# Kernel tuning notes

Measured on AMD Instinct MI355X. Metric: run time of the kernel, lower is better.

The kernel has to match this reference:

```python
import jax, jax.numpy as jnp
import numpy as np

N = 100000   # nodes
E = 1600000  # edges
D = 128      # input feature dim
H = 128      # hidden dim
C = 40       # output classes


def _gcn_conv(x, W, b, src, dst, norm):
    # PyG GCNConv: h = x @ W; out_i = sum_j (d_i^-1/2 d_j^-1/2) h_j over in-edges,
    # including self-loops, then + bias. norm = deg^-1/2 with self-loop-augmented degree.
    h = x @ W                                    # [N, H]
    coef = norm[src] * norm[dst]                 # [E]
    agg = jax.ops.segment_sum(h[src] * coef[:, None], dst, num_segments=N)
    agg = agg + h * (norm * norm)[:, None]       # self-loop term
    return agg + b


def setup_inputs() -> dict:
    key = jax.random.key(0)
    ks = jax.random.split(key, 12)
    x = jax.random.normal(ks[0], (N, D), dtype=jnp.float32)
    edge_index = jax.random.randint(ks[1], (2, E), 0, N, dtype=jnp.int64)

    def lin(k, fan_in, fan_out):
        s = 1.0 / np.sqrt(fan_in)
        return jax.random.uniform(k, (fan_in, fan_out), jnp.float32, -s, s)

    return {
        "x": x,
        "edge_index": edge_index,
        "W1": lin(ks[2], D, H), "b1": jnp.zeros((H,), jnp.float32),
        "W2": lin(ks[3], H, H), "b2": jnp.zeros((H,), jnp.float32),
        "W3": lin(ks[4], H, H), "b3": jnp.zeros((H,), jnp.float32),
        "Wp1": lin(ks[5], H, H), "bp1": jnp.zeros((H,), jnp.float32),
        "Wp2": lin(ks[6], H, C), "bp2": jnp.zeros((C,), jnp.float32),
    }


def reference(x, edge_index, W1, b1, W2, b2, W3, b3, Wp1, bp1, Wp2, bp2):
    src, dst = edge_index[0], edge_index[1]
    # degree with self-loops (GCNConv adds self-loops by default)
    deg = jax.ops.segment_sum(jnp.ones((E,), jnp.float32), dst, num_segments=N) + 1.0
    norm = jax.lax.rsqrt(deg)                    # deg^-1/2

    h = x
    for W, b in ((W1, b1), (W2, b2), (W3, b3)):
        h = _gcn_conv(h, W, b, src, dst, norm)
        h = jax.nn.relu(h)
        # dropout is a no-op at inference / rate 0

    h = h @ Wp1 + bp1
    h = h @ Wp2 + bp2
    return jax.nn.log_softmax(h, axis=1)
```

## Files before the change

kernel.cpp:

```cpp
#include <hip/hip_runtime.h>
#include <hip/hip_bf16.h>
#include <math.h>


#define DH 128
#define NC 40
#define BN 128
#define MAXNB 1024
#define CAP 2560
#define CH 4096
#define SP 136
#define NPREP (3 * DH * DH + 48 * DH + 48)

typedef __attribute__((ext_vector_type(8))) short bf16x8;
typedef __attribute__((ext_vector_type(4))) float f32x4;

__device__ __forceinline__ unsigned short f2bf(float f) {
    unsigned u = __float_as_uint(f);
    unsigned r = (u + 0x7fffu + ((u >> 16) & 1u)) >> 16;
    return (unsigned short)r;
}
__device__ __forceinline__ unsigned pack2(float lo, float hi) {
    return (unsigned)f2bf(lo) | ((unsigned)f2bf(hi) << 16);
}


__global__ __launch_bounds__(256) void bucket_scatter_prep(
        const int* __restrict__ src, const int* __restrict__ dst, int E,
        unsigned* __restrict__ bpos, unsigned* __restrict__ ebuf,
        const float* __restrict__ W1, const float* __restrict__ W2,
        const float* __restrict__ W3, const float* __restrict__ Wp1,
        const float* __restrict__ bp1, const float* __restrict__ Wp2,
        const float* __restrict__ bp2, unsigned short* __restrict__ Wt,
        unsigned short* __restrict__ Wft, float* __restrict__ bfh, int gC) {
    __shared__ unsigned hist[MAXNB];
    __shared__ unsigned gbase[MAXNB];
    __shared__ unsigned lim[MAXNB];
    __shared__ unsigned cur[MAXNB];
    const int tid = threadIdx.x;

    if (blockIdx.x >= gC) {
        int id = (blockIdx.x - gC) * 256 + tid;
        if (id < 3 * DH * DH) {
            int l = id >> 14, r = id & (DH * DH - 1);
            int k = r >> 7, n = r & 127;
            const float* W = (l == 0) ? W1 : (l == 1) ? W2 : W3;
            Wt[l * DH * DH + n * DH + k] = f2bf(W[k * DH + n]);
        } else if (id < 3 * DH * DH + 48 * DH) {
            int o = id - 3 * DH * DH;
            int c = o >> 7, k = o & 127;
            float acc = 0.f;
            if (c < NC)
                for (int j = 0; j < DH; ++j) acc += Wp1[k * DH + j] * Wp2[j * NC + c];
            Wft[c * DH + k] = f2bf(acc);
        } else if (id < NPREP) {
            int c = id - 3 * DH * DH - 48 * DH;
            float acc = 0.f;
            if (c < NC) {
                acc = bp2[c];
                for (int j = 0; j < DH; ++j) acc += bp1[j] * Wp2[j * NC + c];
            }
            bfh[c] = acc;
        }
        return;
    }

    const int e0 = blockIdx.x * CH;
    const int nE = min(CH, E - e0);
    const int nE4 = nE & ~3;

    for (int i = tid; i < MAXNB; i += 256) { hist[i] = 0; cur[i] = 0; }
    __syncthreads();
    for (int i = tid * 4; i < nE4; i += 1024) {
        int4 dv = *(const int4*)(dst + e0 + i);
        atomicAdd(&hist[(unsigned)dv.x >> 7], 1u);
        atomicAdd(&hist[(unsigned)dv.y >> 7], 1u);
        atomicAdd(&hist[(unsigned)dv.z >> 7], 1u);
        atomicAdd(&hist[(unsigned)dv.w >> 7], 1u);
    }
    for (int i = nE4 + tid; i < nE; i += 256)
        atomicAdd(&hist[(unsigned)dst[e0 + i] >> 7], 1u);
    __syncthreads();
    for (int i = tid; i < MAXNB; i += 256) {
        unsigned h = hist[i];
        if (h) {
            unsigned o = (unsigned)i * CAP + atomicAdd(&bpos[i], h);
            gbase[i] = o;
            lim[i] = min(o + h, (unsigned)(i + 1) * CAP);
        }
    }
    __syncthreads();
    for (int i = tid * 4; i < nE4; i += 1024) {
        int4 sv = *(const int4*)(src + e0 + i);
        int4 dv = *(const int4*)(dst + e0 + i);
        {
            unsigned b = (unsigned)dv.x >> 7;
            unsigned p = gbase[b] + atomicAdd(&cur[b], 1u);
            if (p < lim[b]) ebuf[p] = ((unsigned)sv.x << 7) | ((unsigned)dv.x & 127u);
        }
        {
            unsigned b = (unsigned)dv.y >> 7;
            unsigned p = gbase[b] + atomicAdd(&cur[b], 1u);
            if (p < lim[b]) ebuf[p] = ((unsigned)sv.y << 7) | ((unsigned)dv.y & 127u);
        }
        {
            unsigned b = (unsigned)dv.z >> 7;
            unsigned p = gbase[b] + atomicAdd(&cur[b], 1u);
            if (p < lim[b]) ebuf[p] = ((unsigned)sv.z << 7) | ((unsigned)dv.z & 127u);
        }
        {
            unsigned b = (unsigned)dv.w >> 7;
            unsigned p = gbase[b] + atomicAdd(&cur[b], 1u);
            if (p < lim[b]) ebuf[p] = ((unsigned)sv.w << 7) | ((unsigned)dv.w & 127u);
        }
    }
    for (int i = nE4 + tid; i < nE; i += 256) {
        int s = src[e0 + i];
        int d = dst[e0 + i];
        unsigned b = (unsigned)d >> 7;
        unsigned p = gbase[b] + atomicAdd(&cur[b], 1u);
        if (p < lim[b]) ebuf[p] = ((unsigned)s << 7) | ((unsigned)d & 127u);
    }
}


__global__ __launch_bounds__(256) void bucket_degfill(const unsigned* __restrict__ ebuf,
                                                      const unsigned* __restrict__ bpos,
                                                      unsigned* __restrict__ cnt,
                                                      float* __restrict__ nrm,
                                                      unsigned* __restrict__ offN,
                                                      unsigned* __restrict__ dh,
                                                      int* __restrict__ csr, int N) {
    __shared__ unsigned h[BN], lb[BN], cur[BN];
    __shared__ int lcsr[CAP];
    __shared__ unsigned dhh[256];
    __shared__ unsigned tot;

    int b = blockIdx.x, tid = threadIdx.x;
    unsigned ebase = (unsigned)b * CAP;
    unsigned used = min(bpos[b], (unsigned)CAP);
    unsigned used4 = used & ~3u;

    if (tid < BN) { h[tid] = 0; cur[tid] = 0; }
    dhh[tid] = 0;
    if (tid == 0) tot = 0;
    __syncthreads();

    for (unsigned i = tid * 4; i < used4; i += 1024) {
        uint4 v = *(const uint4*)(ebuf + ebase + i);
        atomicAdd(&h[v.x & 127u], 1u);
        atomicAdd(&h[v.y & 127u], 1u);
        atomicAdd(&h[v.z & 127u], 1u);
        atomicAdd(&h[v.w & 127u], 1u);
    }
    for (unsigned i = used4 + tid; i < used; i += 256)
        atomicAdd(&h[ebuf[ebase + i] & 127u], 1u);
    __syncthreads();

    if (tid < BN) {
        unsigned m = h[tid];
        lb[tid] = m ? atomicAdd(&tot, m) : 0u;
    }
    __syncthreads();

    for (unsigned i = tid * 4; i < used4; i += 1024) {
        uint4 v = *(const uint4*)(ebuf + ebase + i);
        {
            unsigned nl = v.x & 127u;
            unsigned r = atomicAdd(&cur[nl], 1u);
            lcsr[lb[nl] + r] = (int)(v.x >> 7);
        }
        {
            unsigned nl = v.y & 127u;
            unsigned r = atomicAdd(&cur[nl], 1u);
            lcsr[lb[nl] + r] = (int)(v.y >> 7);
        }
        {
            unsigned nl = v.z & 127u;
            unsigned r = atomicAdd(&cur[nl], 1u);
            lcsr[lb[nl] + r] = (int)(v.z >> 7);
        }
        {
            unsigned nl = v.w & 127u;
            unsigned r = atomicAdd(&cur[nl], 1u);
            lcsr[lb[nl] + r] = (int)(v.w >> 7);
        }
    }
    for (unsigned i = used4 + tid; i < used; i += 256) {
        unsigned v = ebuf[ebase + i];
        unsigned nl = v & 127u;
        unsigned r = atomicAdd(&cur[nl], 1u);
        lcsr[lb[nl] + r] = (int)(v >> 7);
    }

    if (tid < BN) {
        int node = b * BN + tid;
        if (node < N) {
            unsigned m = h[tid];
            cnt[node] = m;
            nrm[node] = rsqrtf((float)m + 1.0f);
            offN[node] = ebase + lb[tid];
            atomicAdd(&dhh[min(m, 255u)], 1u);
        }
    }
    __syncthreads();

    for (unsigned i = tid * 4; i < used4; i += 1024)
        *(int4*)(csr + ebase + i) = *(const int4*)&lcsr[i];
    for (unsigned i = used4 + tid; i < used; i += 256)
        csr[ebase + i] = lcsr[i];
    if (dhh[tid]) atomicAdd(&dh[tid], dhh[tid]);
}


__global__ __launch_bounds__(256) void degscat_gemm(
        const unsigned* __restrict__ cnt, int N,
        const unsigned* __restrict__ dh, unsigned* __restrict__ binpos,
        const unsigned* __restrict__ offN, int* __restrict__ perm,
        unsigned* __restrict__ pd2,
        const float* __restrict__ X, const unsigned short* __restrict__ Wt,
        const float* __restrict__ nrm, unsigned short* __restrict__ outb,
        int gG) {
    __shared__ unsigned hh[256], base[256], cur[256], sdh[256], sns[256];
    const int tid = threadIdx.x;

    if (blockIdx.x >= (unsigned)gG) {
        int t = tid;
        hh[t] = 0; cur[t] = 0; sdh[t] = dh[t];
        __syncthreads();
        unsigned ns = 0;
        for (int d = t + 1; d < 256; ++d) ns += sdh[d];
        sns[t] = ns;
        int i = (blockIdx.x - gG) * 256 + t;
        unsigned d = 0;
        if (i < N) { d = min(cnt[i], 255u); atomicAdd(&hh[d], 1u); }
        __syncthreads();
        if (hh[t]) base[t] = sns[t] + atomicAdd(&binpos[t], hh[t]);
        __syncthreads();
        if (i < N) {
            unsigned r = atomicAdd(&cur[d], 1u);
            unsigned idx = base[d] + r;
            perm[idx] = i;
            pd2[idx] = (offN[i] << 9) | min(cnt[i], 511u);
        }
        return;
    }

    const int wave = tid >> 6;
    const int lane = tid & 63;
    const int m = lane & 15;
    const int quad = lane >> 4;
    const int rbase = blockIdx.x * 64 + wave * 16;

    union U8 { bf16x8 v; unsigned u[4]; };

    f32x4 acc[8];
#pragma unroll
    for (int ct = 0; ct < 8; ++ct) acc[ct] = (f32x4){0.f, 0.f, 0.f, 0.f};

#pragma unroll
    for (int kt = 0; kt < 4; ++kt) {
        const int kof = kt * 32 + quad * 8;
        int r = rbase + m;
        r = (r < N) ? r : (N - 1);
        const float* p = X + (size_t)r * DH + kof;
        float4 u0 = *(const float4*)p;
        float4 u1 = *(const float4*)(p + 4);
        U8 t;
        t.u[0] = pack2(u0.x, u0.y);
        t.u[1] = pack2(u0.z, u0.w);
        t.u[2] = pack2(u1.x, u1.y);
        t.u[3] = pack2(u1.z, u1.w);
        bf16x8 a = t.v;
        bf16x8 b[8];
#pragma unroll
        for (int ct = 0; ct < 8; ++ct)
            b[ct] = *(const bf16x8*)(Wt + (ct * 16 + m) * DH + kof);
#pragma unroll
        for (int ct = 0; ct < 8; ++ct)
            acc[ct] = __builtin_amdgcn_mfma_f32_16x16x32_bf16(a, b[ct], acc[ct], 0, 0, 0);
    }

#pragma unroll
    for (int reg = 0; reg < 4; ++reg) {
        int r = rbase + quad * 4 + reg;
        if (r < N) {
            float s = nrm[r];
#pragma unroll
            for (int ct = 0; ct < 8; ++ct)
                outb[(size_t)r * DH + ct * 16 + m] = f2bf(acc[ct][reg] * s);
        }
    }
}


__device__ __forceinline__ void bf8_add(float* acc, uint4 v) {
    acc[0] += __uint_as_float(v.x << 16);
    acc[1] += __uint_as_float(v.x & 0xffff0000u);
    acc[2] += __uint_as_float(v.y << 16);
    acc[3] += __uint_as_float(v.y & 0xffff0000u);
    acc[4] += __uint_as_float(v.z << 16);
    acc[5] += __uint_as_float(v.z & 0xffff0000u);
    acc[6] += __uint_as_float(v.w << 16);
    acc[7] += __uint_as_float(v.w & 0xffff0000u);
}

__device__ __forceinline__ void gather_phase(const uint4* __restrict__ Abf,
                                             const int* __restrict__ csr,
                                             const unsigned* __restrict__ pd2,
                                             const int* __restrict__ perm,
                                             const float* __restrict__ bias,
                                             unsigned short (*sA)[SP],
                                             int* snode, float* snrm, int N) {
    const int tid = threadIdx.x;
    const int g = tid >> 4;
    const int lane = tid & 15;
    const int idx = blockIdx.x * 16 + g;
    if (idx < N) {
        const unsigned pd = pd2[idx];
        const unsigned o = pd >> 9;
        const unsigned d = pd & 511u;
        const int node = perm[idx];

        int i0 = 0, i1 = 0, i2 = 0, i3 = 0;
        if ((unsigned)lane < d)        i0 = csr[o + lane];
        if ((unsigned)(16 + lane) < d) i1 = csr[o + 16 + lane];
        if ((unsigned)(32 + lane) < d) i2 = csr[o + 32 + lane];
        if ((unsigned)(48 + lane) < d) i3 = csr[o + 48 + lane];

        float acc[8];
        {
            uint4 v = Abf[(size_t)node * 16 + lane];
            acc[0] = __uint_as_float(v.x << 16);
            acc[1] = __uint_as_float(v.x & 0xffff0000u);
            acc[2] = __uint_as_float(v.y << 16);
            acc[3] = __uint_as_float(v.y & 0xffff0000u);
            acc[4] = __uint_as_float(v.z << 16);
            acc[5] = __uint_as_float(v.z & 0xffff0000u);
            acc[6] = __uint_as_float(v.w << 16);
            acc[7] = __uint_as_float(v.w & 0xffff0000u);
        }

        const unsigned dl = min(d, 64u);
        const int sb = g << 4;
        unsigned e = 0;
        for (; e + 4 <= dl; e += 4) {
            int rsel = (e < 16) ? i0 : (e < 32) ? i1 : (e < 48) ? i2 : i3;
            int bb = sb + (int)(e & 15u);
            int s0 = __shfl(rsel, bb + 0);
            int s1 = __shfl(rsel, bb + 1);
            int s2 = __shfl(rsel, bb + 2);
            int s3 = __shfl(rsel, bb + 3);
            uint4 v0 = Abf[(size_t)s0 * 16 + lane];
            uint4 v1 = Abf[(size_t)s1 * 16 + lane];
            uint4 v2 = Abf[(size_t)s2 * 16 + lane];
            uint4 v3 = Abf[(size_t)s3 * 16 + lane];
            bf8_add(acc, v0);
            bf8_add(acc, v1);
            bf8_add(acc, v2);
            bf8_add(acc, v3);
        }
        for (; e < dl; ++e) {
            int rsel = (e < 16) ? i0 : (e < 32) ? i1 : (e < 48) ? i2 : i3;
            int s = __shfl(rsel, sb + (int)(e & 15u));
            uint4 v = Abf[(size_t)s * 16 + lane];
            bf8_add(acc, v);
        }
        for (; e < d; ++e) {
            int s = csr[o + e];
            uint4 v = Abf[(size_t)s * 16 + lane];
            bf8_add(acc, v);
        }

        float nm = rsqrtf((float)d + 1.0f);
        if (lane == 0) { snode[g] = node; snrm[g] = nm; }
        float4 b0 = *(const float4*)(bias + lane * 8);
        float4 b1 = *(const float4*)(bias + lane * 8 + 4);
        uint4 ov;
        ov.x = pack2(fmaxf(acc[0] * nm + b0.x, 0.f), fmaxf(acc[1] * nm + b0.y, 0.f));
        ov.y = pack2(fmaxf(acc[2] * nm + b0.z, 0.f), fmaxf(acc[3] * nm + b0.w, 0.f));
        ov.z = pack2(fmaxf(acc[4] * nm + b1.x, 0.f), fmaxf(acc[5] * nm + b1.y, 0.f));
        ov.w = pack2(fmaxf(acc[6] * nm + b1.z, 0.f), fmaxf(acc[7] * nm + b1.w, 0.f));
        *(uint4*)&sA[g][lane * 8] = ov;
    }
    __syncthreads();
}


__global__ __launch_bounds__(256) void agg_gemm(const uint4* __restrict__ Abf,
                                                const int* __restrict__ csr,
                                                const unsigned* __restrict__ pd2,
                                                const int* __restrict__ perm,
                                                const float* __restrict__ bias,
                                                const unsigned short* __restrict__ Wt,
                                                unsigned short* __restrict__ outb, int N) {
    __shared__ unsigned short sA[16][SP];
    __shared__ int snode[16];
    __shared__ float snrm[16];
    gather_phase(Abf, csr, pd2, perm, bias, sA, snode, snrm, N);

    const int tid = threadIdx.x;
    const int wave = tid >> 6;
    const int l64 = tid & 63;
    const int m = l64 & 15;
    const int quad = l64 >> 4;

    f32x4 acc[2];
    acc[0] = (f32x4){0.f, 0.f, 0.f, 0.f};
    acc[1] = (f32x4){0.f, 0.f, 0.f, 0.f};

#pragma unroll
    for (int kt = 0; kt < 4; ++kt) {
        const int kof = kt * 32 + quad * 8;
        bf16x8 a = *(const bf16x8*)&sA[m][kof];
#pragma unroll
        for (int c2 = 0; c2 < 2; ++c2) {
            const int ct = wave * 2 + c2;
            bf16x8 b = *(const bf16x8*)(Wt + (ct * 16 + m) * DH + kof);
            acc[c2] = __builtin_amdgcn_mfma_f32_16x16x32_bf16(a, b, acc[c2], 0, 0, 0);
        }
    }

#pragma unroll
    for (int reg = 0; reg < 4; ++reg) {
        int idx = blockIdx.x * 16 + quad * 4 + reg;
        if (idx < N) {
            int r = snode[quad * 4 + reg];
            float s = snrm[quad * 4 + reg];
#pragma unroll
            for (int c2 = 0; c2 < 2; ++c2)
                outb[(size_t)r * DH + (wave * 2 + c2) * 16 + m] = f2bf(acc[c2][reg] * s);
        }
    }
}


__global__ __launch_bounds__(256) void agg_head(const uint4* __restrict__ Abf,
                                                const int* __restrict__ csr,
                                                const unsigned* __restrict__ pd2,
                                                const int* __restrict__ perm,
                                                const float* __restrict__ bias,
                                                const unsigned short* __restrict__ Wft,
                                                const float* __restrict__ bfh,
                                                float* __restrict__ out, int N) {
    __shared__ unsigned short sA[16][SP];
    __shared__ int snode[16];
    __shared__ float snrm[16];
    gather_phase(Abf, csr, pd2, perm, bias, sA, snode, snrm, N);

    const int tid = threadIdx.x;
    if (tid >= 64) return;
    const int m = tid & 15;
    const int quad = tid >> 4;

    f32x4 acc[3];
#pragma unroll
    for (int ct = 0; ct < 3; ++ct) acc[ct] = (f32x4){0.f, 0.f, 0.f, 0.f};

#pragma unroll
    for (int kt = 0; kt < 4; ++kt) {
        const int kof = kt * 32 + quad * 8;
        bf16x8 a = *(const bf16x8*)&sA[m][kof];
#pragma unroll
        for (int ct = 0; ct < 3; ++ct) {
            bf16x8 b = *(const bf16x8*)(Wft + (ct * 16 + m) * DH + kof);
            acc[ct] = __builtin_amdgcn_mfma_f32_16x16x32_bf16(a, b, acc[ct], 0, 0, 0);
        }
    }

    float bias0 = bfh[m];
    float bias1 = bfh[16 + m];
    float bias2 = bfh[32 + m];

#pragma unroll
    for (int reg = 0; reg < 4; ++reg) {
        float v0 = acc[0][reg] + bias0;
        float v1 = acc[1][reg] + bias1;
        float v2 = (m < 8) ? (acc[2][reg] + bias2) : -1e30f;
        float mx = fmaxf(fmaxf(v0, v1), v2);
#pragma unroll
        for (int dlt = 1; dlt < 16; dlt <<= 1) mx = fmaxf(mx, __shfl_xor(mx, dlt));
        float s = __expf(v0 - mx) + __expf(v1 - mx) + ((m < 8) ? __expf(v2 - mx) : 0.f);
#pragma unroll
        for (int dlt = 1; dlt < 16; dlt <<= 1) s += __shfl_xor(s, dlt);
        float ls = mx + __logf(s);
        int idx = blockIdx.x * 16 + quad * 4 + reg;
        if (idx < N) {
            int r = snode[quad * 4 + reg];
            out[(size_t)r * NC + m] = v0 - ls;
            out[(size_t)r * NC + 16 + m] = v1 - ls;
            if (m < 8) out[(size_t)r * NC + 32 + m] = v2 - ls;
        }
    }
}


extern "C" void kernel_launch(void* const* d_in, const int* in_sizes, int n_in,
                              void* d_out, int out_size, void* d_ws, size_t ws_size,
                              hipStream_t stream) {
    const float* x   = (const float*)d_in[0];
    const int*   ei  = (const int*)d_in[1];
    const float* W1  = (const float*)d_in[2];
    const float* b1  = (const float*)d_in[3];
    const float* W2  = (const float*)d_in[4];
    const float* b2  = (const float*)d_in[5];
    const float* W3  = (const float*)d_in[6];
    const float* b3  = (const float*)d_in[7];
    const float* Wp1 = (const float*)d_in[8];
    const float* bp1 = (const float*)d_in[9];
    const float* Wp2 = (const float*)d_in[10];
    const float* bp2 = (const float*)d_in[11];
    float* out = (float*)d_out;

    const int N = in_sizes[0] / DH;
    const int E = in_sizes[1] / 2;
    const int* src = ei;
    const int* dst = ei + E;
    const int NB = (N + BN - 1) / BN;

    char* w = (char*)d_ws;
    unsigned short* Ab  = (unsigned short*)w; w += (size_t)N * DH * 2;
    unsigned short* Bb  = (unsigned short*)w; w += (size_t)N * DH * 2;
    int*      csr    = (int*)w;      w += (size_t)NB * CAP * 4;
    unsigned* ebuf   = (unsigned*)w; w += (size_t)NB * CAP * 4;
    unsigned* dh     = (unsigned*)w; w += 256 * 4;
    unsigned* binpos = (unsigned*)w; w += 256 * 4;
    unsigned* bpos   = (unsigned*)w; w += MAXNB * 4;
    unsigned* cnt    = (unsigned*)w; w += (size_t)N * 4;
    float*    nrm    = (float*)w;    w += (size_t)N * 4;
    unsigned* offN   = (unsigned*)w; w += (size_t)N * 4;
    unsigned* pd2    = (unsigned*)w; w += (size_t)((N + 31) & ~31) * 4;
    int*      perm   = (int*)w;      w += (size_t)((N + 31) & ~31) * 4;
    unsigned short* Wt  = (unsigned short*)w; w += 3 * DH * DH * 2;
    unsigned short* Wft = (unsigned short*)w; w += 48 * DH * 2;
    float*    bfh    = (float*)w;    w += 64 * 4;

    const int gC = (E + CH - 1) / CH;
    const int gN = (N + 255) / 256;
    const int gP = (NPREP + 255) / 256;
    const int gG = (N + 63) / 64;
    const int gF = (N + 15) / 16;

    hipMemsetAsync(dh, 0, 256 * 4 + 256 * 4 + MAXNB * 4, stream);
    bucket_scatter_prep<<<gC + gP, 256, 0, stream>>>(src, dst, E, bpos, ebuf,
                                                     W1, W2, W3, Wp1, bp1, Wp2, bp2,
                                                     Wt, Wft, bfh, gC);
    bucket_degfill<<<NB, 256, 0, stream>>>(ebuf, bpos, cnt, nrm, offN, dh, csr, N);
    degscat_gemm<<<gG + gN, 256, 0, stream>>>(cnt, N, dh, binpos, offN, perm, pd2,
                                              x, Wt, nrm, Ab, gG);

    agg_gemm<<<gF, 256, 0, stream>>>((const uint4*)Ab, csr, pd2, perm, b1,
                                     Wt + DH * DH, Bb, N);
    agg_gemm<<<gF, 256, 0, stream>>>((const uint4*)Bb, csr, pd2, perm, b2,
                                     Wt + 2 * DH * DH, Ab, N);
    agg_head<<<gF, 256, 0, stream>>>((const uint4*)Ab, csr, pd2, perm, b3,
                                     Wft, bfh, out, N);
}
```

Before: 370.4 us.

## Split features into column slabs and separate gather from GEMM kernels

```diff
diff --git a/kernel.cpp b/kernel.cpp
--- a/kernel.cpp
+++ b/kernel.cpp
@@ -9,7 +9,6 @@
 #define MAXNB 1024
 #define CAP 2560
 #define CH 4096
-#define SP 136
 #define NPREP (3 * DH * DH + 48 * DH + 48)
 
 typedef __attribute__((ext_vector_type(8))) short bf16x8;
@@ -288,170 +287,142 @@
             float s = nrm[r];
 #pragma unroll
             for (int ct = 0; ct < 8; ++ct)
-                outb[(size_t)r * DH + ct * 16 + m] = f2bf(acc[ct][reg] * s);
-        }
-    }
-}
-
-
-__device__ __forceinline__ void bf8_add(float* acc, uint4 v) {
-    acc[0] += __uint_as_float(v.x << 16);
-    acc[1] += __uint_as_float(v.x & 0xffff0000u);
-    acc[2] += __uint_as_float(v.y << 16);
-    acc[3] += __uint_as_float(v.y & 0xffff0000u);
-    acc[4] += __uint_as_float(v.z << 16);
-    acc[5] += __uint_as_float(v.z & 0xffff0000u);
-    acc[6] += __uint_as_float(v.w << 16);
-    acc[7] += __uint_as_float(v.w & 0xffff0000u);
-}
-
-__device__ __forceinline__ void gather_phase(const uint4* __restrict__ Abf,
-                                             const int* __restrict__ csr,
-                                             const unsigned* __restrict__ pd2,
-                                             const int* __restrict__ perm,
-                                             const float* __restrict__ bias,
-                                             unsigned short (*sA)[SP],
-                                             int* snode, float* snrm, int N) {
+                outb[((size_t)ct * N + r) * 16 + m] = f2bf(acc[ct][reg] * s);
+        }
+    }
+}
+
+
+__global__ __launch_bounds__(256) void gather_slab(
+        const unsigned* __restrict__ Abs, const int* __restrict__ csr,
+        const unsigned* __restrict__ pd2, const int* __restrict__ perm,
+        const float* __restrict__ bias, unsigned* __restrict__ Hs,
+        int N, int nchunk) {
     const int tid = threadIdx.x;
-    const int g = tid >> 4;
-    const int lane = tid & 15;
-    const int idx = blockIdx.x * 16 + g;
-    if (idx < N) {
-        const unsigned pd = pd2[idx];
-        const unsigned o = pd >> 9;
-        const unsigned d = pd & 511u;
-        const int node = perm[idx];
-
-        int i0 = 0, i1 = 0, i2 = 0, i3 = 0;
-        if ((unsigned)lane < d)        i0 = csr[o + lane];
-        if ((unsigned)(16 + lane) < d) i1 = csr[o + 16 + lane];
-        if ((unsigned)(32 + lane) < d) i2 = csr[o + 32 + lane];
-        if ((unsigned)(48 + lane) < d) i3 = csr[o + 48 + lane];
-
-        float acc[8];
-        {
-            uint4 v = Abf[(size_t)node * 16 + lane];
-            acc[0] = __uint_as_float(v.x << 16);
-            acc[1] = __uint_as_float(v.x & 0xffff0000u);
-            acc[2] = __uint_as_float(v.y << 16);
-            acc[3] = __uint_as_float(v.y & 0xffff0000u);
-            acc[4] = __uint_as_float(v.z << 16);
-            acc[5] = __uint_as_float(v.z & 0xffff0000u);
-            acc[6] = __uint_as_float(v.w << 16);
-            acc[7] = __uint_as_float(v.w & 0xffff0000u);
-        }
-
-        const unsigned dl = min(d, 64u);
-        const int sb = g << 4;
-        unsigned e = 0;
-        for (; e + 4 <= dl; e += 4) {
-            int rsel = (e < 16) ? i0 : (e < 32) ? i1 : (e < 48) ? i2 : i3;
-            int bb = sb + (int)(e & 15u);
-            int s0 = __shfl(rsel, bb + 0);
-            int s1 = __shfl(rsel, bb + 1);
-            int s2 = __shfl(rsel, bb + 2);
-            int s3 = __shfl(rsel, bb + 3);
-            uint4 v0 = Abf[(size_t)s0 * 16 + lane];
-            uint4 v1 = Abf[(size_t)s1 * 16 + lane];
-            uint4 v2 = Abf[(size_t)s2 * 16 + lane];
-            uint4 v3 = Abf[(size_t)s3 * 16 + lane];
-            bf8_add(acc, v0);
-            bf8_add(acc, v1);
-            bf8_add(acc, v2);
-            bf8_add(acc, v3);
-        }
-        for (; e < dl; ++e) {
-            int rsel = (e < 16) ? i0 : (e < 32) ? i1 : (e < 48) ? i2 : i3;
-            int s = __shfl(rsel, sb + (int)(e & 15u));
-            uint4 v = Abf[(size_t)s * 16 + lane];
-            bf8_add(acc, v);
-        }
-        for (; e < d; ++e) {
-            int s = csr[o + e];
-            uint4 v = Abf[(size_t)s * 16 + lane];
-            bf8_add(acc, v);
-        }
-
-        float nm = rsqrtf((float)d + 1.0f);
-        if (lane == 0) { snode[g] = node; snrm[g] = nm; }
-        float4 b0 = *(const float4*)(bias + lane * 8);
-        float4 b1 = *(const float4*)(bias + lane * 8 + 4);
-        uint4 ov;
-        ov.x = pack2(fmaxf(acc[0] * nm + b0.x, 0.f), fmaxf(acc[1] * nm + b0.y, 0.f));
-        ov.y = pack2(fmaxf(acc[2] * nm + b0.z, 0.f), fmaxf(acc[3] * nm + b0.w, 0.f));
-        ov.z = pack2(fmaxf(acc[4] * nm + b1.x, 0.f), fmaxf(acc[5] * nm + b1.y, 0.f));
-        ov.w = pack2(fmaxf(acc[6] * nm + b1.z, 0.f), fmaxf(acc[7] * nm + b1.w, 0.f));
-        *(uint4*)&sA[g][lane * 8] = ov;
-    }
-    __syncthreads();
-}
-
-
-__global__ __launch_bounds__(256) void agg_gemm(const uint4* __restrict__ Abf,
-                                                const int* __restrict__ csr,
-                                                const unsigned* __restrict__ pd2,
-                                                const int* __restrict__ perm,
-                                                const float* __restrict__ bias,
-                                                const unsigned short* __restrict__ Wt,
-                                                unsigned short* __restrict__ outb, int N) {
-    __shared__ unsigned short sA[16][SP];
-    __shared__ int snode[16];
-    __shared__ float snrm[16];
-    gather_phase(Abf, csr, pd2, perm, bias, sA, snode, snrm, N);
-
+    const int slab = blockIdx.x & 7;
+    const int g = tid >> 3;
+    const int l2 = tid & 7;
+    const int sb = ((tid & 63) >> 3) << 3;
+
+    const size_t sbase = (size_t)slab * (unsigned)N;
+    const float2 bv = *(const float2*)(bias + slab * 16 + l2 * 2);
+
+    for (int chunk = blockIdx.x >> 3; chunk < nchunk; chunk += 256) {
+        const int pbase = chunk * 256 + g * 8;
+#pragma unroll 1
+        for (int t = 0; t < 8; ++t) {
+            const int idx = pbase + t;
+            if (idx >= N) break;
+            const unsigned pd = pd2[idx];
+            const unsigned o = pd >> 9;
+            const unsigned d = pd & 511u;
+            const int node = perm[idx];
+
+            int i0 = 0, i1 = 0, i2 = 0, i3 = 0;
+            if ((unsigned)l2 < d)        i0 = csr[o + l2];
+            if ((unsigned)(8 + l2) < d)  i1 = csr[o + 8 + l2];
+            if ((unsigned)(16 + l2) < d) i2 = csr[o + 16 + l2];
+            if ((unsigned)(24 + l2) < d) i3 = csr[o + 24 + l2];
+
+            unsigned sv = Abs[(sbase + (unsigned)node) * 8 + l2];
+            float a0 = __uint_as_float(sv << 16);
+            float a1 = __uint_as_float(sv & 0xffff0000u);
+
+            const unsigned dl = min(d, 32u);
+            unsigned e = 0;
+            for (; e + 4 <= dl; e += 4) {
+                int rsel = (e < 8) ? i0 : (e < 16) ? i1 : (e < 24) ? i2 : i3;
+                int bb = sb + (int)(e & 7u);
+                int s0 = __shfl(rsel, bb + 0);
+                int s1 = __shfl(rsel, bb + 1);
+                int s2 = __shfl(rsel, bb + 2);
+                int s3 = __shfl(rsel, bb + 3);
+                unsigned v0 = Abs[(sbase + (unsigned)s0) * 8 + l2];
+                unsigned v1 = Abs[(sbase + (unsigned)s1) * 8 + l2];
+                unsigned v2 = Abs[(sbase + (unsigned)s2) * 8 + l2];
+                unsigned v3 = Abs[(sbase + (unsigned)s3) * 8 + l2];
+                a0 += __uint_as_float(v0 << 16); a1 += __uint_as_float(v0 & 0xffff0000u);
+                a0 += __uint_as_float(v1 << 16); a1 += __uint_as_float(v1 & 0xffff0000u);
+                a0 += __uint_as_float(v2 << 16); a1 += __uint_as_float(v2 & 0xffff0000u);
+                a0 += __uint_as_float(v3 << 16); a1 += __uint_as_float(v3 & 0xffff0000u);
+            }
+            for (; e < dl; ++e) {
+                int rsel = (e < 8) ? i0 : (e < 16) ? i1 : (e < 24) ? i2 : i3;
+                int s0 = __shfl(rsel, sb + (int)(e & 7u));
+                unsigned v = Abs[(sbase + (unsigned)s0) * 8 + l2];
+                a0 += __uint_as_float(v << 16); a1 += __uint_as_float(v & 0xffff0000u);
+            }
+            for (; e < d; ++e) {
+                int s0 = csr[o + e];
+                unsigned v = Abs[(sbase + (unsigned)s0) * 8 + l2];
+                a0 += __uint_as_float(v << 16); a1 += __uint_as_float(v & 0xffff0000u);
+            }
+
+            float nm = rsqrtf((float)d + 1.0f);
+            Hs[(sbase + (unsigned)node) * 8 + l2] =
+                pack2(fmaxf(a0 * nm + bv.x, 0.f), fmaxf(a1 * nm + bv.y, 0.f));
+        }
+    }
+}
+
+
+__global__ __launch_bounds__(256) void gemm_slab(
+        const unsigned short* __restrict__ Hs,
+        const unsigned short* __restrict__ Wt,
+        const float* __restrict__ nrm,
+        unsigned short* __restrict__ outb, int N) {
     const int tid = threadIdx.x;
     const int wave = tid >> 6;
-    const int l64 = tid & 63;
-    const int m = l64 & 15;
-    const int quad = l64 >> 4;
-
-    f32x4 acc[2];
-    acc[0] = (f32x4){0.f, 0.f, 0.f, 0.f};
-    acc[1] = (f32x4){0.f, 0.f, 0.f, 0.f};
+    const int lane = tid & 63;
+    const int m = lane & 15;
+    const int quad = lane >> 4;
+    const int rbase = blockIdx.x * 64 + wave * 16;
+
+    f32x4 acc[8];
+#pragma unroll
+    for (int ct = 0; ct < 8; ++ct) acc[ct] = (f32x4){0.f, 0.f, 0.f, 0.f};
 
 #pragma unroll
     for (int kt = 0; kt < 4; ++kt) {
         const int kof = kt * 32 + quad * 8;
-        bf16x8 a = *(const bf16x8*)&sA[m][kof];
-#pragma unroll
-        for (int c2 = 0; c2 < 2; ++c2) {
-            const int ct = wave * 2 + c2;
-            bf16x8 b = *(const bf16x8*)(Wt + (ct * 16 + m) * DH + kof);
-            acc[c2] = __builtin_amdgcn_mfma_f32_16x16x32_bf16(a, b, acc[c2], 0, 0, 0);
-        }
+        const int slab = kof >> 4;
+        const int koff = kof & 15;
+        int r = rbase + m;
+        r = (r < N) ? r : (N - 1);
+        bf16x8 a = *(const bf16x8*)(Hs + ((size_t)slab * N + r) * 16 + koff);
+        bf16x8 b[8];
+#pragma unroll
+        for (int ct = 0; ct < 8; ++ct)
+            b[ct] = *(const bf16x8*)(Wt + (ct * 16 + m) * DH + kof);
+#pragma unroll
+        for (int ct = 0; ct < 8; ++ct)
+            acc[ct] = __builtin_amdgcn_mfma_f32_16x16x32_bf16(a, b[ct], acc[ct], 0, 0, 0);
     }
 
 #pragma unroll
     for (int reg = 0; reg < 4; ++reg) {
-        int idx = blockIdx.x * 16 + quad * 4 + reg;
-        if (idx < N) {
-            int r = snode[quad * 4 + reg];
-            float s = snrm[quad * 4 + reg];
-#pragma unroll
-            for (int c2 = 0; c2 < 2; ++c2)
-                outb[(size_t)r * DH + (wave * 2 + c2) * 16 + m] = f2bf(acc[c2][reg] * s);
-        }
-    }
-}
-
-
-__global__ __launch_bounds__(256) void agg_head(const uint4* __restrict__ Abf,
-                                                const int* __restrict__ csr,
-                                                const unsigned* __restrict__ pd2,
-                                                const int* __restrict__ perm,
-                                                const float* __restrict__ bias,
-                                                const unsigned short* __restrict__ Wft,
-                                                const float* __restrict__ bfh,
-                                                float* __restrict__ out, int N) {
-    __shared__ unsigned short sA[16][SP];
-    __shared__ int snode[16];
-    __shared__ float snrm[16];
-    gather_phase(Abf, csr, pd2, perm, bias, sA, snode, snrm, N);
-
+        int r = rbase + quad * 4 + reg;
+        if (r < N) {
+            float s = nrm[r];
+#pragma unroll
+            for (int ct = 0; ct < 8; ++ct)
+                outb[((size_t)ct * N + r) * 16 + m] = f2bf(acc[ct][reg] * s);
+        }
+    }
+}
+
+
+__global__ __launch_bounds__(256) void head_slab(
+        const unsigned short* __restrict__ Hs,
+        const unsigned short* __restrict__ Wft,
+        const float* __restrict__ bfh,
+        float* __restrict__ out, int N) {
     const int tid = threadIdx.x;
-    if (tid >= 64) return;
-    const int m = tid & 15;
-    const int quad = tid >> 4;
+    const int wave = tid >> 6;
+    const int lane = tid & 63;
+    const int m = lane & 15;
+    const int quad = lane >> 4;
+    const int rbase = blockIdx.x * 64 + wave * 16;
 
     f32x4 acc[3];
 #pragma unroll
@@ -460,7 +431,11 @@
 #pragma unroll
     for (int kt = 0; kt < 4; ++kt) {
         const int kof = kt * 32 + quad * 8;
-        bf16x8 a = *(const bf16x8*)&sA[m][kof];
+        const int slab = kof >> 4;
+        const int koff = kof & 15;
+        int r = rbase + m;
+        r = (r < N) ? r : (N - 1);
+        bf16x8 a = *(const bf16x8*)(Hs + ((size_t)slab * N + r) * 16 + koff);
 #pragma unroll
         for (int ct = 0; ct < 3; ++ct) {
             bf16x8 b = *(const bf16x8*)(Wft + (ct * 16 + m) * DH + kof);
@@ -484,9 +459,8 @@
 #pragma unroll
         for (int dlt = 1; dlt < 16; dlt <<= 1) s += __shfl_xor(s, dlt);
         float ls = mx + __logf(s);
-        int idx = blockIdx.x * 16 + quad * 4 + reg;
-        if (idx < N) {
-            int r = snode[quad * 4 + reg];
+        int r = rbase + quad * 4 + reg;
+        if (r < N) {
             out[(size_t)r * NC + m] = v0 - ls;
             out[(size_t)r * NC + 16 + m] = v1 - ls;
             if (m < 8) out[(size_t)r * NC + 32 + m] = v2 - ls;
@@ -539,7 +513,7 @@
     const int gN = (N + 255) / 256;
     const int gP = (NPREP + 255) / 256;
     const int gG = (N + 63) / 64;
-    const int gF = (N + 15) / 16;
+    const int nchunk = (N + 255) / 256;
 
     hipMemsetAsync(dh, 0, 256 * 4 + 256 * 4 + MAXNB * 4, stream);
     bucket_scatter_prep<<<gC + gP, 256, 0, stream>>>(src, dst, E, bpos, ebuf,
@@ -549,10 +523,13 @@
     degscat_gemm<<<gG + gN, 256, 0, stream>>>(cnt, N, dh, binpos, offN, perm, pd2,
                                               x, Wt, nrm, Ab, gG);
 
-    agg_gemm<<<gF, 256, 0, stream>>>((const uint4*)Ab, csr, pd2, perm, b1,
-                                     Wt + DH * DH, Bb, N);
-    agg_gemm<<<gF, 256, 0, stream>>>((const uint4*)Bb, csr, pd2, perm, b2,
-                                     Wt + 2 * DH * DH, Ab, N);
-    agg_head<<<gF, 256, 0, stream>>>((const uint4*)Ab, csr, pd2, perm, b3,
-                                     Wft, bfh, out, N);
-}
+    gather_slab<<<2048, 256, 0, stream>>>((const unsigned*)Ab, csr, pd2, perm, b1,
+                                          (unsigned*)Bb, N, nchunk);
+    gemm_slab<<<gG, 256, 0, stream>>>(Bb, Wt + DH * DH, nrm, Ab, N);
+    gather_slab<<<2048, 256, 0, stream>>>((const unsigned*)Ab, csr, pd2, perm, b2,
+                                          (unsigned*)Bb, N, nchunk);
+    gemm_slab<<<gG, 256, 0, stream>>>(Bb, Wt + 2 * DH * DH, nrm, Ab, N);
+    gather_slab<<<2048, 256, 0, stream>>>((const unsigned*)Ab, csr, pd2, perm, b3,
+                                          (unsigned*)Bb, N, nchunk);
+    head_slab<<<gG, 256, 0, stream>>>(Bb, Wft, bfh, out, N);
+}
```

New measurement: 599.5 us. 1.62x slower.
